# Performance work log

Measured on AMD Instinct MI355X. Metric: run time of the kernel, lower is better.

## Reference

```python
import jax, jax.numpy as jnp
import numpy as np

N_NODES = 100000
BN_EPS = 1e-5


def _gcn_layer(x, W, b, row, col, ew):
    # support = x @ W  (dense GEMM), then sparse aggregation: out[r] += w * support[c]
    support = x @ W
    msgs = ew[:, None] * support[col]            # [E, out_dim] gather
    agg = jax.ops.segment_sum(msgs, row, num_segments=N_NODES)
    return agg + b


def _batch_norm(x):
    # fresh BatchNorm1d each call: training-mode batch stats, gamma=1, beta=0
    mean = jnp.mean(x, axis=0, keepdims=True)
    var = jnp.var(x, axis=0, keepdims=True)      # biased variance, as in BN
    return (x - mean) * jax.lax.rsqrt(var + BN_EPS)


def setup_inputs() -> dict:
    key = jax.random.key(0)
    ks = jax.random.split(key, 10)
    nfeat, nhid, nclass = 512, 256, 64
    E = 3200000
    x = jax.random.normal(ks[0], (N_NODES, nfeat), dtype=jnp.float32)
    edge_index = jax.random.randint(ks[1], (2, E), 0, N_NODES, dtype=jnp.int32)
    edge_weight = jax.random.uniform(ks[2], (E,), dtype=jnp.float32)
    def glorot(k, fan_in, fan_out):
        s = 1.0 / np.sqrt(fan_in)
        return jax.random.uniform(k, (fan_in, fan_out), dtype=jnp.float32, minval=-s, maxval=s)
    W1 = glorot(ks[3], nfeat, nhid)
    b1 = jnp.zeros((nhid,), dtype=jnp.float32)
    W2 = glorot(ks[4], nhid, nhid)
    b2 = jnp.zeros((nhid,), dtype=jnp.float32)
    W3 = glorot(ks[5], nhid, nclass)
    b3 = jnp.zeros((nclass,), dtype=jnp.float32)
    return {"x": x, "edge_index": edge_index, "edge_weight": edge_weight,
            "W1": W1, "b1": b1, "W2": W2, "b2": b2, "W3": W3, "b3": b3}


def reference(x, edge_index, edge_weight, W1, b1, W2, b2, W3, b3):
    row, col = edge_index[0], edge_index[1]
    h = _batch_norm(jax.nn.relu(_gcn_layer(x, W1, b1, row, col, edge_weight)))
    h = _batch_norm(jax.nn.relu(_gcn_layer(h, W2, b2, row, col, edge_weight)))
    h = jax.nn.relu(_gcn_layer(h, W3, b3, row, col, edge_weight))
    return h
```

## Files before the change

### kernel.cpp

```cpp
#include <hip/hip_runtime.h>

#define THREADS 256
#define BSH 8
#define EPB 8192

typedef _Float16 f16;
typedef _Float16 f16x8 __attribute__((ext_vector_type(8)));
typedef _Float16 f16x4 __attribute__((ext_vector_type(4)));
typedef _Float16 f16x2 __attribute__((ext_vector_type(2)));
typedef float f32x4 __attribute__((ext_vector_type(4)));


__global__ void k_scan1(const int* __restrict__ cnt, int* __restrict__ outp,
                        int* __restrict__ bsum, int n) {
  __shared__ int sh[256];
  int t = threadIdx.x;
  int base = blockIdx.x * 1024 + t * 4;
  int v[4];
#pragma unroll
  for (int j = 0; j < 4; ++j) {
    int idx = base + j;
    v[j] = (idx < n) ? cnt[idx] : 0;
  }
  int tot = v[0] + v[1] + v[2] + v[3];
  sh[t] = tot;
  __syncthreads();
  for (int off = 1; off < 256; off <<= 1) {
    int x = 0;
    if (t >= off) x = sh[t - off];
    __syncthreads();
    sh[t] += x;
    __syncthreads();
  }
  if (t == 255) bsum[blockIdx.x] = sh[255];
  int run = sh[t] - tot;
#pragma unroll
  for (int j = 0; j < 4; ++j) {
    int idx = base + j;
    if (idx < n) outp[idx] = run;
    run += v[j];
  }
}

__global__ void k_scan2(int* __restrict__ bsum, int nb) {
  __shared__ int sh[256];
  int t = threadIdx.x;
  int v = (t < nb) ? bsum[t] : 0;
  sh[t] = v;
  __syncthreads();
  for (int off = 1; off < 256; off <<= 1) {
    int x = 0;
    if (t >= off) x = sh[t - off];
    __syncthreads();
    sh[t] += x;
    __syncthreads();
  }
  if (t < nb) bsum[t] = sh[t] - v;
}

__global__ void k_scan3(int* __restrict__ outp, const int* __restrict__ bsum,
                        int n, int total) {
  int base = blockIdx.x * 1024 + threadIdx.x * 4;
  int add = bsum[blockIdx.x];
#pragma unroll
  for (int j = 0; j < 4; ++j) {
    int idx = base + j;
    if (idx < n) outp[idx] += add;
  }
  if (blockIdx.x == 0 && threadIdx.x == 0) outp[n] = total;
}


__global__ __launch_bounds__(256) void k_hist(const int* __restrict__ rows,
                                              int* __restrict__ cnt2d,
                                              int e, int nblk, int nb) {
  __shared__ int hist[512];
  int blk = blockIdx.x, t = threadIdx.x;
  for (int i = t; i < nb; i += 256) hist[i] = 0;
  __syncthreads();
  int eb = blk * EPB;
#pragma unroll 4
  for (int it = 0; it < 32; ++it) {
    int i = eb + it * 256 + t;
    if (i < e) atomicAdd(&hist[rows[i] >> BSH], 1);
  }
  __syncthreads();
  for (int i = t; i < nb; i += 256) cnt2d[i * nblk + blk] = hist[i];
}

__global__ __launch_bounds__(256) void k_bin(
    const int* __restrict__ rows, const int* __restrict__ cols,
    const float* __restrict__ w, const int* __restrict__ off2d,
    int2* __restrict__ temp, int e, int nblk, int nb) {
  __shared__ int base[512];
  __shared__ int cursor[512];
  int blk = blockIdx.x, t = threadIdx.x;
  for (int i = t; i < nb; i += 256) {
    base[i] = off2d[i * nblk + blk];
    cursor[i] = 0;
  }
  __syncthreads();
  int eb = blk * EPB;
#pragma unroll 4
  for (int it = 0; it < 32; ++it) {
    int i = eb + it * 256 + t;
    if (i < e) {
      int r = rows[i];
      int b = r >> BSH;
      int pos = base[b] + atomicAdd(&cursor[b], 1);
      temp[pos] = make_int2(((r & 255) << 17) | cols[i], __float_as_int(w[i]));
    }
  }
}

__global__ __launch_bounds__(256) void k_scatter(
    const int2* __restrict__ temp, const int* __restrict__ off2d,
    int* __restrict__ rowptr, int2* __restrict__ ed,
    int n, int e, int nblk, int nb) {
  __shared__ int rowCnt[256];
  __shared__ int rowBase[256];
  __shared__ int rowCur[256];
  int b = blockIdx.x, t = threadIdx.x;
  int r0 = b << BSH;
  int nr = min(256, n - r0);
  int start = off2d[b * nblk];
  int end = off2d[(b + 1) * nblk];
  rowCnt[t] = 0;
  __syncthreads();
  for (int p = start + t; p < end; p += 256)
    atomicAdd(&rowCnt[temp[p].x >> 17], 1);
  __syncthreads();
  int v = rowCnt[t];
  rowBase[t] = v;
  __syncthreads();
  for (int off = 1; off < 256; off <<= 1) {
    int x = 0;
    if (t >= off) x = rowBase[t - off];
    __syncthreads();
    rowBase[t] += x;
    __syncthreads();
  }
  int excl = rowBase[t] - v;
  __syncthreads();
  rowBase[t] = excl;
  rowCur[t] = 0;
  if (t < nr) rowptr[r0 + t] = start + excl;
  if (b == nb - 1 && t == 0) rowptr[n] = e;
  __syncthreads();
  for (int p = start + t; p < end; p += 256) {
    int2 ei = temp[p];
    int ro = ei.x >> 17;
    int slot = start + rowBase[ro] + atomicAdd(&rowCur[ro], 1);
    ed[slot] = make_int2(ei.x & 0x1FFFF, ei.y);
  }
}


__global__ void k_convW(const float* __restrict__ W, f16* __restrict__ Wt, int K, int N,
                        float* __restrict__ statZero) {
  int i = blockIdx.x * THREADS + threadIdx.x;
  if (blockIdx.x == 0) {
#pragma unroll
    for (int j = 0; j < 6; ++j) statZero[j * 256 + threadIdx.x] = 0.f;
  }
  if (i >= N * K) return;
  int n = i / K, k = i - n * K;
  Wt[i] = (f16)W[(size_t)k * N + n];
}

__global__ __launch_bounds__(256) void k_bnfold(
    const float* __restrict__ W, const float* __restrict__ sums,
    f16* __restrict__ Wt, float* __restrict__ biasRow, int K, int N, int n) {
  __shared__ float sc[256], sf[256];
  int t = threadIdx.x;
  if (t < K) {
    float inv = 1.0f / (float)n;
    float mean = sums[t] * inv;
    float var = sums[256 + t] * inv - mean * mean;
    float rstd = rsqrtf(var + 1e-5f);
    sc[t] = rstd;
    sf[t] = -mean * rstd;
  }
  __syncthreads();
  int i = blockIdx.x * 256 + t;
  if (i < N * K) {
    int nn = i / K, k = i - nn * K;
    Wt[i] = (f16)(sc[k] * W[(size_t)k * N + nn]);
  }
  if (blockIdx.x < (K >> 4) && t < N) {
    int k0 = blockIdx.x * 16;
    float s = 0.f;
#pragma unroll
    for (int j = 0; j < 16; ++j) s += sf[k0 + j] * W[(size_t)(k0 + j) * N + t];
    atomicAdd(&biasRow[t], s);
  }
}


template <int BN, bool AF16>
__global__ __launch_bounds__(256) void k_gemm_mfma(
    const void* __restrict__ Ap, const f16* __restrict__ Wt,
    const float* __restrict__ biasRow, f16* __restrict__ Csup, int M, int K) {
  constexpr int BM = 128;
  constexpr int BK = 32;
  constexpr int LDT = BK + 8;
  __shared__ __align__(16) f16 As[BM][LDT];
  __shared__ __align__(16) f16 Bs[BN][LDT];

  const int tid = threadIdx.x;
  const int wave = tid >> 6;
  const int lane = tid & 63;
  const int m0 = blockIdx.x * BM;
  constexpr int WM = (BN == 256) ? 8 : 2;
  constexpr int WN = 4;
  const int wrow = (BN == 256) ? 0 : wave * 32;
  const int wcol = (BN == 256) ? wave * 64 : 0;
  const int l15 = lane & 15;
  const int lq = lane >> 4;

  const int arow = tid >> 1;
  const int akofs = (tid & 1) * 16;
  const int srow = tid >> 2;
  const int skofs = (tid & 3) * 8;
  constexpr int BROWS = BN / 64;

  f32x4 acc[WM][WN] = {};

  for (int k0 = 0; k0 < K; k0 += BK) {
    f16x8 a16[2];
    int gr = m0 + arow;
    if constexpr (AF16) {
      if (gr < M) {
        const f16* ap = (const f16*)Ap + (size_t)gr * K + k0 + akofs;
        a16[0] = *(const f16x8*)ap;
        a16[1] = *(const f16x8*)(ap + 8);
      } else {
#pragma unroll
        for (int j = 0; j < 8; ++j) { a16[0][j] = (f16)0.f; a16[1][j] = (f16)0.f; }
      }
    } else {
      float va[16];
      if (gr < M) {
        const float* ap = (const float*)Ap + (size_t)gr * K + k0 + akofs;
#pragma unroll
        for (int q = 0; q < 4; ++q) *(float4*)&va[q * 4] = *(const float4*)(ap + q * 4);
      } else {
#pragma unroll
        for (int j = 0; j < 16; ++j) va[j] = 0.f;
      }
#pragma unroll
      for (int j = 0; j < 8; ++j) { a16[0][j] = (f16)va[j]; a16[1][j] = (f16)va[8 + j]; }
    }

    f16x8 vb[BROWS];
#pragma unroll
    for (int j = 0; j < BROWS; ++j)
      vb[j] = *(const f16x8*)(Wt + (size_t)(srow + j * 64) * K + k0 + skofs);

    __syncthreads();
    *(f16x8*)&As[arow][akofs] = a16[0];
    *(f16x8*)&As[arow][akofs + 8] = a16[1];
#pragma unroll
    for (int j = 0; j < BROWS; ++j) *(f16x8*)&Bs[srow + j * 64][skofs] = vb[j];
    __syncthreads();

    f16x8 af[WM], bf[WN];
#pragma unroll
    for (int m = 0; m < WM; ++m)
      af[m] = *(const f16x8*)&As[wrow + m * 16 + l15][lq * 8];
#pragma unroll
    for (int n = 0; n < WN; ++n)
      bf[n] = *(const f16x8*)&Bs[wcol + n * 16 + l15][lq * 8];
#pragma unroll
    for (int m = 0; m < WM; ++m)
#pragma unroll
      for (int n = 0; n < WN; ++n)
        acc[m][n] = __builtin_amdgcn_mfma_f32_16x16x32_f16(af[m], bf[n], acc[m][n], 0, 0, 0);
  }

  float bb[WN];
#pragma unroll
  for (int n = 0; n < WN; ++n)
    bb[n] = biasRow ? biasRow[wcol + n * 16 + l15] : 0.f;

#pragma unroll
  for (int m = 0; m < WM; ++m) {
#pragma unroll
    for (int r = 0; r < 4; ++r) {
      int row = m0 + wrow + m * 16 + lq * 4 + r;
      if (row < M) {
        f16* cp = Csup + (size_t)row * BN + wcol + l15;
#pragma unroll
        for (int n = 0; n < WN; ++n) cp[n * 16] = (f16)(acc[m][n][r] + bb[n]);
      }
    }
  }
}


__global__ __launch_bounds__(256) void k_agg256(
    const f16* __restrict__ sup, const int* __restrict__ rowptr,
    const int2* __restrict__ ed, const float* __restrict__ bias,
    f16* __restrict__ out, int n) {
  int wid = (blockIdx.x * THREADS + threadIdx.x) >> 6;
  int lane = threadIdx.x & 63;
  if (wid >= n) return;
  int p0 = rowptr[wid], p1 = rowptr[wid + 1];

  const f16x4* supv = (const f16x4*)sup;
  float acc[4][4] = {};
  int p = p0;
  for (; p + 16 <= p1; p += 16) {
    int2 e[16];
#pragma unroll
    for (int j = 0; j < 16; ++j) e[j] = ed[p + j];
    f16x4 v[16];
#pragma unroll
    for (int j = 0; j < 16; ++j) v[j] = supv[(size_t)e[j].x * 64 + lane];
#pragma unroll
    for (int j = 0; j < 16; ++j) {
      float wt = __int_as_float(e[j].y);
      acc[j & 3][0] += wt * (float)v[j][0];
      acc[j & 3][1] += wt * (float)v[j][1];
      acc[j & 3][2] += wt * (float)v[j][2];
      acc[j & 3][3] += wt * (float)v[j][3];
    }
  }
  for (; p + 4 <= p1; p += 4) {
    int2 e[4];
#pragma unroll
    for (int j = 0; j < 4; ++j) e[j] = ed[p + j];
    f16x4 v[4];
#pragma unroll
    for (int j = 0; j < 4; ++j) v[j] = supv[(size_t)e[j].x * 64 + lane];
#pragma unroll
    for (int j = 0; j < 4; ++j) {
      float wt = __int_as_float(e[j].y);
      acc[j][0] += wt * (float)v[j][0];
      acc[j][1] += wt * (float)v[j][1];
      acc[j][2] += wt * (float)v[j][2];
      acc[j][3] += wt * (float)v[j][3];
    }
  }
  for (; p < p1; ++p) {
    int2 e0 = ed[p];
    float wt = __int_as_float(e0.y);
    f16x4 v = supv[(size_t)e0.x * 64 + lane];
    acc[0][0] += wt * (float)v[0];
    acc[0][1] += wt * (float)v[1];
    acc[0][2] += wt * (float)v[2];
    acc[0][3] += wt * (float)v[3];
  }
  float4 b = *(const float4*)(bias + lane * 4);
  f16x4 r;
  r[0] = (f16)fmaxf(acc[0][0] + acc[1][0] + acc[2][0] + acc[3][0] + b.x, 0.f);
  r[1] = (f16)fmaxf(acc[0][1] + acc[1][1] + acc[2][1] + acc[3][1] + b.y, 0.f);
  r[2] = (f16)fmaxf(acc[0][2] + acc[1][2] + acc[2][2] + acc[3][2] + b.z, 0.f);
  r[3] = (f16)fmaxf(acc[0][3] + acc[1][3] + acc[2][3] + acc[3][3] + b.w, 0.f);
  *(f16x4*)(out + (size_t)wid * 256 + lane * 4) = r;
}


__global__ __launch_bounds__(256) void k_agg64(
    const f16* __restrict__ sup, const int* __restrict__ rowptr,
    const int2* __restrict__ ed, const float* __restrict__ bias,
    float* __restrict__ out, int n) {
  int wid = (blockIdx.x * THREADS + threadIdx.x) >> 6;
  int lane = threadIdx.x & 63;
  if (wid >= n) return;
  int p0 = rowptr[wid], p1 = rowptr[wid + 1];
  int half = lane >> 5;
  int hl = lane & 31;

  const f16x2* supv = (const f16x2*)sup;
  float ax = 0.f, ay = 0.f, bx = 0.f, by = 0.f;
  int p = p0;
  for (; p + 32 <= p1; p += 32) {
    int2 e[16];
#pragma unroll
    for (int j = 0; j < 16; ++j) e[j] = ed[p + 2 * j + half];
    f16x2 v[16];
#pragma unroll
    for (int j = 0; j < 16; ++j) v[j] = supv[(size_t)e[j].x * 32 + hl];
#pragma unroll
    for (int j = 0; j < 16; ++j) {
      float wt = __int_as_float(e[j].y);
      if (j & 1) { bx += wt * (float)v[j][0]; by += wt * (float)v[j][1]; }
      else       { ax += wt * (float)v[j][0]; ay += wt * (float)v[j][1]; }
    }
  }
  for (; p + 8 <= p1; p += 8) {
    int2 e[4];
#pragma unroll
    for (int j = 0; j < 4; ++j) e[j] = ed[p + 2 * j + half];
    f16x2 v[4];
#pragma unroll
    for (int j = 0; j < 4; ++j) v[j] = supv[(size_t)e[j].x * 32 + hl];
#pragma unroll
    for (int j = 0; j < 4; ++j) {
      float wt = __int_as_float(e[j].y);
      if (j & 1) { bx += wt * (float)v[j][0]; by += wt * (float)v[j][1]; }
      else       { ax += wt * (float)v[j][0]; ay += wt * (float)v[j][1]; }
    }
  }
  for (; p < p1; p += 2) {
    int idx = p + half;
    float wt = 0.f;
    int c = 0;
    if (idx < p1) {
      int2 e0 = ed[idx];
      c = e0.x;
      wt = __int_as_float(e0.y);
    }
    f16x2 v = supv[(size_t)c * 32 + hl];
    ax += wt * (float)v[0];
    ay += wt * (float)v[1];
  }
  float tx = ax + bx;
  float ty = ay + by;
  tx += __shfl_xor(tx, 32);
  ty += __shfl_xor(ty, 32);
  if (half == 0) {
    float2 b = *(const float2*)(bias + hl * 2);
    float2 res;
    res.x = fmaxf(tx + b.x, 0.f);
    res.y = fmaxf(ty + b.y, 0.f);
    *(float2*)(out + (size_t)wid * 64 + hl * 2) = res;
  }
}


__global__ __launch_bounds__(256) void k_colstats(const f16* __restrict__ y,
                                                  float* __restrict__ sums, int n) {
  __shared__ float sh[8][256];
  int t = threadIdx.x;
  int cg = (t & 31) * 8;
  int rs = t >> 5;
  float s[8] = {}, s2[8] = {};
  for (int r = blockIdx.x * 8 + rs; r < n; r += gridDim.x * 8) {
    f16x8 v = *(const f16x8*)(y + (size_t)r * 256 + cg);
#pragma unroll
    for (int j = 0; j < 8; ++j) {
      float f = (float)v[j];
      s[j] += f;
      s2[j] += f * f;
    }
  }
#pragma unroll
  for (int j = 0; j < 8; ++j) sh[rs][cg + j] = s[j];
  __syncthreads();
  float tot = 0.f;
#pragma unroll
  for (int k = 0; k < 8; ++k) tot += sh[k][t];
  atomicAdd(&sums[t], tot);
  __syncthreads();
#pragma unroll
  for (int j = 0; j < 8; ++j) sh[rs][cg + j] = s2[j];
  __syncthreads();
  tot = 0.f;
#pragma unroll
  for (int k = 0; k < 8; ++k) tot += sh[k][t];
  atomicAdd(&sums[256 + t], tot);
}


extern "C" void kernel_launch(void* const* d_in, const int* in_sizes, int n_in,
                              void* d_out, int out_size, void* d_ws, size_t ws_size,
                              hipStream_t stream) {
  const float* x = (const float*)d_in[0];
  const int* ei = (const int*)d_in[1];
  const float* ew = (const float*)d_in[2];
  const float* W1 = (const float*)d_in[3];
  const float* b1 = (const float*)d_in[4];
  const float* W2 = (const float*)d_in[5];
  const float* b2 = (const float*)d_in[6];
  const float* W3 = (const float*)d_in[7];
  const float* b3 = (const float*)d_in[8];
  float* out = (float*)d_out;

  const int N = in_sizes[0] / 512;
  const int E = in_sizes[2];

  const int NB = (N + 255) >> BSH;
  const int NBLK = (E + EPB - 1) / EPB;
  const int scanN = NB * NBLK;

  char* p = (char*)d_ws;
  auto alloc = [&](size_t bytes) {
    void* r = (void*)p;
    p += (bytes + 255) & ~(size_t)255;
    return r;
  };
  int* rowptr = (int*)alloc((size_t)(N + 1) * 4);
  int* cnt2d = (int*)alloc((size_t)scanN * 4);
  int* off2d = (int*)alloc((size_t)(scanN + 1) * 4);
  int* bsum = (int*)alloc(4096);
  float* statZ = (float*)alloc(1536 * 4);
  float* sumsA = statZ;
  float* sumsB = statZ + 512;
  float* biasRowA = statZ + 1024;
  float* biasRowB = statZ + 1280;
  f16* Wt1 = (f16*)alloc((size_t)512 * 256 * 2);
  f16* Wt2 = (f16*)alloc((size_t)256 * 256 * 2);
  f16* Wt3 = (f16*)alloc((size_t)256 * 64 * 2);
  int2* temp = (int2*)alloc((size_t)E * 8);
  int2* ed = (int2*)alloc((size_t)E * 8);
  f16* sup = (f16*)alloc((size_t)N * 256 * 2);
  f16* act = (f16*)alloc((size_t)N * 256 * 2);

  const int* rows = ei;
  const int* colsIn = ei + E;

  k_hist<<<NBLK, 256, 0, stream>>>(rows, cnt2d, E, NBLK, NB);
  int nbs = (scanN + 1023) / 1024;
  k_scan1<<<nbs, 256, 0, stream>>>(cnt2d, off2d, bsum, scanN);
  k_scan2<<<1, 256, 0, stream>>>(bsum, nbs);
  k_scan3<<<nbs, 256, 0, stream>>>(off2d, bsum, scanN, E);
  k_bin<<<NBLK, 256, 0, stream>>>(rows, colsIn, ew, off2d, temp, E, NBLK, NB);
  k_scatter<<<NB, 256, 0, stream>>>(temp, off2d, rowptr, ed, N, E, NBLK, NB);

  const int gemmBlocks = (N + 127) / 128;
  const int aggBlocks = (N * 64 + THREADS - 1) / THREADS;

  k_convW<<<(512 * 256 + THREADS - 1) / THREADS, THREADS, 0, stream>>>(W1, Wt1, 512, 256, statZ);
  k_gemm_mfma<256, false><<<gemmBlocks, 256, 0, stream>>>(x, Wt1, nullptr, sup, N, 512);
  k_agg256<<<aggBlocks, 256, 0, stream>>>(sup, rowptr, ed, b1, act, N);

  k_colstats<<<240, 256, 0, stream>>>(act, sumsA, N);
  k_bnfold<<<(256 * 256 + 255) / 256, 256, 0, stream>>>(W2, sumsA, Wt2, biasRowA, 256, 256, N);

  k_gemm_mfma<256, true><<<gemmBlocks, 256, 0, stream>>>(act, Wt2, biasRowA, sup, N, 256);
  k_agg256<<<aggBlocks, 256, 0, stream>>>(sup, rowptr, ed, b2, act, N);

  k_colstats<<<240, 256, 0, stream>>>(act, sumsB, N);
  k_bnfold<<<(256 * 64 + 255) / 256, 256, 0, stream>>>(W3, sumsB, Wt3, biasRowB, 256, 64, N);

  k_gemm_mfma<64, true><<<gemmBlocks, 256, 0, stream>>>(act, Wt3, biasRowB, sup, N, 256);
  k_agg64<<<aggBlocks, 256, 0, stream>>>(sup, rowptr, ed, b3, out, N);
}
```

Before: 883.8 us.

## Use nontemporal edge loads, widen agg64 lanes, fuse weight conversion into histogram

Edge records are now read with nontemporal loads so the streamed edge list pollutes the cache less, leaving more room for the gathered support rows. The 64-wide aggregation now has four lane groups each process one edge with f16x4 loads, instead of two groups with f16x2 loads, reduced by two shuffles. The first weight transpose/convert kernel is merged into the histogram launch as extra blocks, saving one launch. Risks include the nontemporal hint being ineffective or harmful, and a larger shuffle reduction.

```diff
diff --git a/kernel.cpp b/kernel.cpp
--- a/kernel.cpp
+++ b/kernel.cpp
@@ -9,6 +9,13 @@
 typedef _Float16 f16x4 __attribute__((ext_vector_type(4)));
 typedef _Float16 f16x2 __attribute__((ext_vector_type(2)));
 typedef float f32x4 __attribute__((ext_vector_type(4)));
+
+__device__ __forceinline__ void nt_edge(const int2* ed, int idx, int& c, float& wt) {
+  unsigned long long v =
+      __builtin_nontemporal_load((const unsigned long long*)(ed + idx));
+  c = (int)(v & 0xffffffffull);
+  wt = __int_as_float((int)(v >> 32));
+}
 
 
 __global__ void k_scan1(const int* __restrict__ cnt, int* __restrict__ outp,
@@ -71,21 +78,36 @@
 }
 
 
-__global__ __launch_bounds__(256) void k_hist(const int* __restrict__ rows,
-                                              int* __restrict__ cnt2d,
-                                              int e, int nblk, int nb) {
-  __shared__ int hist[512];
-  int blk = blockIdx.x, t = threadIdx.x;
-  for (int i = t; i < nb; i += 256) hist[i] = 0;
-  __syncthreads();
-  int eb = blk * EPB;
+__global__ __launch_bounds__(256) void k_hist_convW(
+    const int* __restrict__ rows, int* __restrict__ cnt2d, int e, int nblk, int nb,
+    const float* __restrict__ W, f16* __restrict__ Wt, int K, int N,
+    float* __restrict__ statZero) {
+  int t = threadIdx.x;
+  if (blockIdx.x < nblk) {
+    __shared__ int hist[512];
+    int blk = blockIdx.x;
+    for (int i = t; i < nb; i += 256) hist[i] = 0;
+    __syncthreads();
+    int eb = blk * EPB;
 #pragma unroll 4
-  for (int it = 0; it < 32; ++it) {
-    int i = eb + it * 256 + t;
-    if (i < e) atomicAdd(&hist[rows[i] >> BSH], 1);
-  }
-  __syncthreads();
-  for (int i = t; i < nb; i += 256) cnt2d[i * nblk + blk] = hist[i];
+    for (int it = 0; it < 32; ++it) {
+      int i = eb + it * 256 + t;
+      if (i < e) atomicAdd(&hist[rows[i] >> BSH], 1);
+    }
+    __syncthreads();
+    for (int i = t; i < nb; i += 256) cnt2d[i * nblk + blk] = hist[i];
+  } else {
+    int cb = blockIdx.x - nblk;
+    if (cb == 0) {
+#pragma unroll
+      for (int j = 0; j < 6; ++j) statZero[j * 256 + t] = 0.f;
+    }
+    int i = cb * 256 + t;
+    if (i < N * K) {
+      int n = i / K, k = i - n * K;
+      Wt[i] = (f16)W[(size_t)k * N + n];
+    }
+  }
 }
 
 __global__ __launch_bounds__(256) void k_bin(
@@ -156,18 +178,6 @@
 }
 
 
-__global__ void k_convW(const float* __restrict__ W, f16* __restrict__ Wt, int K, int N,
-                        float* __restrict__ statZero) {
-  int i = blockIdx.x * THREADS + threadIdx.x;
-  if (blockIdx.x == 0) {
-#pragma unroll
-    for (int j = 0; j < 6; ++j) statZero[j * 256 + threadIdx.x] = 0.f;
-  }
-  if (i >= N * K) return;
-  int n = i / K, k = i - n * K;
-  Wt[i] = (f16)W[(size_t)k * N + n];
-}
-
 __global__ __launch_bounds__(256) void k_bnfold(
     const float* __restrict__ W, const float* __restrict__ sums,
     f16* __restrict__ Wt, float* __restrict__ biasRow, int K, int N, int n) {
@@ -311,41 +321,42 @@
   float acc[4][4] = {};
   int p = p0;
   for (; p + 16 <= p1; p += 16) {
-    int2 e[16];
-#pragma unroll
-    for (int j = 0; j < 16; ++j) e[j] = ed[p + j];
+    int c[16];
+    float wt[16];
+#pragma unroll
+    for (int j = 0; j < 16; ++j) nt_edge(ed, p + j, c[j], wt[j]);
     f16x4 v[16];
 #pragma unroll
-    for (int j = 0; j < 16; ++j) v[j] = supv[(size_t)e[j].x * 64 + lane];
+    for (int j = 0; j < 16; ++j) v[j] = supv[(size_t)c[j] * 64 + lane];
 #pragma unroll
     for (int j = 0; j < 16; ++j) {
-      float wt = __int_as_float(e[j].y);
-      acc[j & 3][0] += wt * (float)v[j][0];
-      acc[j & 3][1] += wt * (float)v[j][1];
-      acc[j & 3][2] += wt * (float)v[j][2];
-      acc[j & 3][3] += wt * (float)v[j][3];
+      acc[j & 3][0] += wt[j] * (float)v[j][0];
+      acc[j & 3][1] += wt[j] * (float)v[j][1];
+      acc[j & 3][2] += wt[j] * (float)v[j][2];
+      acc[j & 3][3] += wt[j] * (float)v[j][3];
     }
   }
   for (; p + 4 <= p1; p += 4) {
-    int2 e[4];
-#pragma unroll
-    for (int j = 0; j < 4; ++j) e[j] = ed[p + j];
+    int c[4];
+    float wt[4];
+#pragma unroll
+    for (int j = 0; j < 4; ++j) nt_edge(ed, p + j, c[j], wt[j]);
     f16x4 v[4];
 #pragma unroll
-    for (int j = 0; j < 4; ++j) v[j] = supv[(size_t)e[j].x * 64 + lane];
+    for (int j = 0; j < 4; ++j) v[j] = supv[(size_t)c[j] * 64 + lane];
 #pragma unroll
     for (int j = 0; j < 4; ++j) {
-      float wt = __int_as_float(e[j].y);
-      acc[j][0] += wt * (float)v[j][0];
-      acc[j][1] += wt * (float)v[j][1];
-      acc[j][2] += wt * (float)v[j][2];
-      acc[j][3] += wt * (float)v[j][3];
+      acc[j][0] += wt[j] * (float)v[j][0];
+      acc[j][1] += wt[j] * (float)v[j][1];
+      acc[j][2] += wt[j] * (float)v[j][2];
+      acc[j][3] += wt[j] * (float)v[j][3];
     }
   }
   for (; p < p1; ++p) {
-    int2 e0 = ed[p];
-    float wt = __int_as_float(e0.y);
-    f16x4 v = supv[(size_t)e0.x * 64 + lane];
+    int c;
+    float wt;
+    nt_edge(ed, p, c, wt);
+    f16x4 v = supv[(size_t)c * 64 + lane];
     acc[0][0] += wt * (float)v[0];
     acc[0][1] += wt * (float)v[1];
     acc[0][2] += wt * (float)v[2];
@@ -369,63 +380,65 @@
   int lane = threadIdx.x & 63;
   if (wid >= n) return;
   int p0 = rowptr[wid], p1 = rowptr[wid + 1];
-  int half = lane >> 5;
-  int hl = lane & 31;
-
-  const f16x2* supv = (const f16x2*)sup;
-  float ax = 0.f, ay = 0.f, bx = 0.f, by = 0.f;
+  int q = lane >> 4;
+  int hl = lane & 15;
+
+  const f16x4* supv = (const f16x4*)sup;
+  float acc[2][4] = {};
   int p = p0;
   for (; p + 32 <= p1; p += 32) {
-    int2 e[16];
-#pragma unroll
-    for (int j = 0; j < 16; ++j) e[j] = ed[p + 2 * j + half];
-    f16x2 v[16];
-#pragma unroll
-    for (int j = 0; j < 16; ++j) v[j] = supv[(size_t)e[j].x * 32 + hl];
-#pragma unroll
-    for (int j = 0; j < 16; ++j) {
-      float wt = __int_as_float(e[j].y);
-      if (j & 1) { bx += wt * (float)v[j][0]; by += wt * (float)v[j][1]; }
-      else       { ax += wt * (float)v[j][0]; ay += wt * (float)v[j][1]; }
-    }
-  }
-  for (; p + 8 <= p1; p += 8) {
-    int2 e[4];
-#pragma unroll
-    for (int j = 0; j < 4; ++j) e[j] = ed[p + 2 * j + half];
-    f16x2 v[4];
-#pragma unroll
-    for (int j = 0; j < 4; ++j) v[j] = supv[(size_t)e[j].x * 32 + hl];
-#pragma unroll
-    for (int j = 0; j < 4; ++j) {
-      float wt = __int_as_float(e[j].y);
-      if (j & 1) { bx += wt * (float)v[j][0]; by += wt * (float)v[j][1]; }
-      else       { ax += wt * (float)v[j][0]; ay += wt * (float)v[j][1]; }
-    }
-  }
-  for (; p < p1; p += 2) {
-    int idx = p + half;
+    int c[8];
+    float wt[8];
+#pragma unroll
+    for (int j = 0; j < 8; ++j) nt_edge(ed, p + 4 * j + q, c[j], wt[j]);
+    f16x4 v[8];
+#pragma unroll
+    for (int j = 0; j < 8; ++j) v[j] = supv[(size_t)c[j] * 16 + hl];
+#pragma unroll
+    for (int j = 0; j < 8; ++j) {
+      acc[j & 1][0] += wt[j] * (float)v[j][0];
+      acc[j & 1][1] += wt[j] * (float)v[j][1];
+      acc[j & 1][2] += wt[j] * (float)v[j][2];
+      acc[j & 1][3] += wt[j] * (float)v[j][3];
+    }
+  }
+  for (; p + 4 <= p1; p += 4) {
+    int c;
+    float wt;
+    nt_edge(ed, p + q, c, wt);
+    f16x4 v = supv[(size_t)c * 16 + hl];
+    acc[0][0] += wt * (float)v[0];
+    acc[0][1] += wt * (float)v[1];
+    acc[0][2] += wt * (float)v[2];
+    acc[0][3] += wt * (float)v[3];
+  }
+  if (p < p1) {
+    int idx = p + q;
+    int c = 0;
     float wt = 0.f;
-    int c = 0;
-    if (idx < p1) {
-      int2 e0 = ed[idx];
-      c = e0.x;
-      wt = __int_as_float(e0.y);
-    }
-    f16x2 v = supv[(size_t)c * 32 + hl];
-    ax += wt * (float)v[0];
-    ay += wt * (float)v[1];
-  }
-  float tx = ax + bx;
-  float ty = ay + by;
-  tx += __shfl_xor(tx, 32);
-  ty += __shfl_xor(ty, 32);
-  if (half == 0) {
-    float2 b = *(const float2*)(bias + hl * 2);
-    float2 res;
-    res.x = fmaxf(tx + b.x, 0.f);
-    res.y = fmaxf(ty + b.y, 0.f);
-    *(float2*)(out + (size_t)wid * 64 + hl * 2) = res;
+    if (idx < p1) nt_edge(ed, idx, c, wt);
+    f16x4 v = supv[(size_t)c * 16 + hl];
+    acc[0][0] += wt * (float)v[0];
+    acc[0][1] += wt * (float)v[1];
+    acc[0][2] += wt * (float)v[2];
+    acc[0][3] += wt * (float)v[3];
+  }
+  float t0 = acc[0][0] + acc[1][0];
+  float t1 = acc[0][1] + acc[1][1];
+  float t2 = acc[0][2] + acc[1][2];
+  float t3 = acc[0][3] + acc[1][3];
+  t0 += __shfl_xor(t0, 16); t0 += __shfl_xor(t0, 32);
+  t1 += __shfl_xor(t1, 16); t1 += __shfl_xor(t1, 32);
+  t2 += __shfl_xor(t2, 16); t2 += __shfl_xor(t2, 32);
+  t3 += __shfl_xor(t3, 16); t3 += __shfl_xor(t3, 32);
+  if (q == 0) {
+    float4 b = *(const float4*)(bias + hl * 4);
+    float4 res;
+    res.x = fmaxf(t0 + b.x, 0.f);
+    res.y = fmaxf(t1 + b.y, 0.f);
+    res.z = fmaxf(t2 + b.z, 0.f);
+    res.w = fmaxf(t3 + b.w, 0.f);
+    *(float4*)(out + (size_t)wid * 64 + hl * 4) = res;
   }
 }
 
@@ -511,7 +524,9 @@
   const int* rows = ei;
   const int* colsIn = ei + E;
 
-  k_hist<<<NBLK, 256, 0, stream>>>(rows, cnt2d, E, NBLK, NB);
+  const int convBlocks = (512 * 256 + 255) / 256;
+  k_hist_convW<<<NBLK + convBlocks, 256, 0, stream>>>(
+      rows, cnt2d, E, NBLK, NB, W1, Wt1, 512, 256, statZ);
   int nbs = (scanN + 1023) / 1024;
   k_scan1<<<nbs, 256, 0, stream>>>(cnt2d, off2d, bsum, scanN);
   k_scan2<<<1, 256, 0, stream>>>(bsum, nbs);
@@ -522,7 +537,6 @@
   const int gemmBlocks = (N + 127) / 128;
   const int aggBlocks = (N * 64 + THREADS - 1) / THREADS;
 
-  k_convW<<<(512 * 256 + THREADS - 1) / THREADS, THREADS, 0, stream>>>(W1, Wt1, 512, 256, statZ);
   k_gemm_mfma<256, false><<<gemmBlocks, 256, 0, stream>>>(x, Wt1, nullptr, sup, N, 512);
   k_agg256<<<aggBlocks, 256, 0, stream>>>(sup, rowptr, ed, b1, act, N);
 
```

Measured after the change: 922.9 us. 1.04x slower.
